# Optimization experiments

Hardware: AMD Instinct MI355X
Metric: run time of the kernel (lower is better)

The kernel has to match this reference:

```python
import jax, jax.numpy as jnp
import numpy as np

L, D, B, S = 131072, 512, 512, 512


def setup_inputs() -> dict:
    key = jax.random.key(0)
    k0, k1, k2, k3 = jax.random.split(key, 4)
    stdv = 1.0 / np.sqrt(D).astype(np.float32)
    inp = jax.random.normal(k0, (B, D), jnp.float32)
    labels = jax.random.normal(k1, (L, D), jnp.float32) * 0.05  # aggregated label embeddings 'v'
    weight = jax.random.uniform(k2, (L, D), jnp.float32, -stdv, stdv)  # refinement vectors 'u'
    alpha = jnp.zeros((1, D), jnp.float32)
    beta = jnp.zeros((1, D), jnp.float32)
    bias = jnp.zeros((L,), jnp.float32)
    shortlist = jax.random.randint(k3, (B, S), 0, L, dtype=jnp.int64)
    return {"input": inp, "labels": labels, "weight": weight,
            "alpha": alpha, "beta": beta, "bias": bias, "shortlist": shortlist}


def reference(input, labels, weight, alpha, beta, bias, shortlist):
    # sigmoid-gated combine of refinement vector u and label embedding v: [L, D]
    lbl_clf = jax.nn.sigmoid(alpha) * weight + jax.nn.sigmoid(beta) * labels
    # shortlist gather: [B, S, D] and [B, S]
    clf = lbl_clf[shortlist]
    b = bias[shortlist]
    # per-sample batched dot products: [B, S]
    out = jnp.einsum('bd,bsd->bs', input, clf) + b
    return out
```

## Files before the change

kernel.cpp:

```cpp
#include <hip/hip_runtime.h>


#define D_DIM 512
#define S_DIM 512

__global__ __launch_bounds__(256, 4)
void combine_uv_kernel(
    const float* __restrict__ input,
    const float* __restrict__ labels,
    const float* __restrict__ weight,
    const float* __restrict__ alpha,
    const float* __restrict__ beta,
    const float* __restrict__ bias,
    const int* __restrict__ shortlist,
    float* __restrict__ out)
{
    __shared__ float ga[D_DIM];
    __shared__ float gb[D_DIM];
    __shared__ int   sl[64];
    __shared__ float bb[64];

    const int b   = blockIdx.x;
    const int s0  = blockIdx.y * 64;
    const int tid = threadIdx.x;

    for (int d = tid; d < D_DIM; d += 256) {
        float x  = input[b * D_DIM + d];
        float sa = 1.0f / (1.0f + __expf(-alpha[d]));
        float sb = 1.0f / (1.0f + __expf(-beta[d]));
        ga[d] = x * sa;
        gb[d] = x * sb;
    }
    if (tid < 64) {
        const int l = shortlist[b * S_DIM + s0 + tid];
        sl[tid] = l;
        bb[tid] = bias[l];
    }
    __syncthreads();

    const int wave = tid >> 6;
    const int lane = tid & 63;
    const int g    = lane >> 4;
    const int m    = lane & 15;

    const float4* gaf = (const float4*)ga;
    const float4* gbf = (const float4*)gb;

    #pragma unroll
    for (int i = 0; i < 4; ++i) {
        const int    si = wave * 16 + i * 4 + g;
        const size_t l  = (size_t)sl[si];
        const float4* wrow = (const float4*)(weight + l * D_DIM);
        const float4* vrow = (const float4*)(labels + l * D_DIM);

        float4 wd[8], vd[8];
        #pragma unroll
        for (int k = 0; k < 8; ++k) wd[k] = wrow[m + 16 * k];
        #pragma unroll
        for (int k = 0; k < 8; ++k) vd[k] = vrow[m + 16 * k];

        float acc = 0.0f;
        #pragma unroll
        for (int k = 0; k < 8; ++k) {
            const float4 a = gaf[m + 16 * k];
            acc += wd[k].x * a.x + wd[k].y * a.y + wd[k].z * a.z + wd[k].w * a.w;
        }
        #pragma unroll
        for (int k = 0; k < 8; ++k) {
            const float4 c = gbf[m + 16 * k];
            acc += vd[k].x * c.x + vd[k].y * c.y + vd[k].z * c.z + vd[k].w * c.w;
        }

        acc += __shfl_xor(acc, 8, 64);
        acc += __shfl_xor(acc, 4, 64);
        acc += __shfl_xor(acc, 2, 64);
        acc += __shfl_xor(acc, 1, 64);

        if (m == 0) out[b * S_DIM + s0 + si] = acc + bb[si];
    }
}

extern "C" void kernel_launch(void* const* d_in, const int* in_sizes, int n_in,
                              void* d_out, int out_size, void* d_ws, size_t ws_size,
                              hipStream_t stream) {
    const float* input     = (const float*)d_in[0];
    const float* labels    = (const float*)d_in[1];
    const float* weight    = (const float*)d_in[2];
    const float* alpha     = (const float*)d_in[3];
    const float* beta      = (const float*)d_in[4];
    const float* bias      = (const float*)d_in[5];
    const int* shortlist   = (const int*)d_in[6];
    float* out             = (float*)d_out;

    const int B = 512;
    const int S = 512;
    dim3 grid(B, S / 64);
    dim3 block(256);
    combine_uv_kernel<<<grid, block, 0, stream>>>(
        input, labels, weight, alpha, beta, bias, shortlist, out);
}
```

Baseline: 567.1 us.

## Invert shortlist gather to label-major order via counting sort for row reuse

Builds a histogram, prefix scan and bucket fill of shortlist entries so each label's weight and label rows are loaded once and reused across every (batch, slot) pair that references them. Sample-major gathers of 4KB rows per pair are replaced by a streaming read over all labels plus gathers of the small precomputed gated-input matrices, which should stay cache-resident. This adds six extra launches, global atomics, workspace usage, and a serial per-wave inner loop with dependent index loads whose latency may limit throughput.

```diff
diff --git a/kernel.cpp b/kernel.cpp
--- a/kernel.cpp
+++ b/kernel.cpp
@@ -1,82 +1,141 @@
 #include <hip/hip_runtime.h>
 
 
+#define L_DIM 131072
 #define D_DIM 512
+#define B_DIM 512
 #define S_DIM 512
+#define NREF  (B_DIM * S_DIM)
 
-__global__ __launch_bounds__(256, 4)
-void combine_uv_kernel(
-    const float* __restrict__ input,
-    const float* __restrict__ labels,
-    const float* __restrict__ weight,
-    const float* __restrict__ alpha,
-    const float* __restrict__ beta,
-    const float* __restrict__ bias,
-    const int* __restrict__ shortlist,
-    float* __restrict__ out)
-{
-    __shared__ float ga[D_DIM];
-    __shared__ float gb[D_DIM];
-    __shared__ int   sl[64];
-    __shared__ float bb[64];
+#define WS_GA     0
+#define WS_GB     (1u << 20)
+#define WS_COUNTS (2u << 20)
+#define WS_STARTS ((2u << 20) + (512u << 10))
+#define WS_CURSOR (3u << 20)
+#define WS_BSUM   ((3u << 20) + (512u << 10))
+#define WS_BOFF   ((3u << 20) + (512u << 10) + 4096)
+#define WS_IDX    (4u << 20)
 
-    const int b   = blockIdx.x;
-    const int s0  = blockIdx.y * 64;
+__global__ void gates_kernel(const float* __restrict__ input,
+                             const float* __restrict__ alpha,
+                             const float* __restrict__ beta,
+                             float* __restrict__ ga, float* __restrict__ gb,
+                             int* __restrict__ counts) {
+    const int b = blockIdx.x, tid = threadIdx.x;
+    for (int d = tid; d < D_DIM; d += 256) {
+        const float x  = input[b * D_DIM + d];
+        const float sa = 1.0f / (1.0f + __expf(-alpha[d]));
+        const float sb = 1.0f / (1.0f + __expf(-beta[d]));
+        ga[b * D_DIM + d] = x * sa;
+        gb[b * D_DIM + d] = x * sb;
+    }
+    counts[b * 256 + tid] = 0;
+}
+
+__global__ void hist_kernel(const int* __restrict__ shortlist, int* __restrict__ counts) {
+    const int i = blockIdx.x * 256 + threadIdx.x;
+    atomicAdd(&counts[shortlist[i]], 1);
+}
+
+__global__ void scan1_kernel(const int* __restrict__ counts, int* __restrict__ bsum) {
+    __shared__ int s[256];
     const int tid = threadIdx.x;
+    s[tid] = counts[blockIdx.x * 256 + tid];
+    __syncthreads();
+    for (int off = 128; off > 0; off >>= 1) {
+        if (tid < off) s[tid] += s[tid + off];
+        __syncthreads();
+    }
+    if (tid == 0) bsum[blockIdx.x] = s[0];
+}
 
-    for (int d = tid; d < D_DIM; d += 256) {
-        float x  = input[b * D_DIM + d];
-        float sa = 1.0f / (1.0f + __expf(-alpha[d]));
-        float sb = 1.0f / (1.0f + __expf(-beta[d]));
-        ga[d] = x * sa;
-        gb[d] = x * sb;
+__global__ void scan2_kernel(const int* __restrict__ bsum, int* __restrict__ boff) {
+    __shared__ int s[512];
+    const int tid = threadIdx.x;
+    const int own = bsum[tid];
+    s[tid] = own;
+    __syncthreads();
+    for (int off = 1; off < 512; off <<= 1) {
+        const int v = (tid >= off) ? s[tid - off] : 0;
+        __syncthreads();
+        s[tid] += v;
+        __syncthreads();
     }
-    if (tid < 64) {
-        const int l = shortlist[b * S_DIM + s0 + tid];
-        sl[tid] = l;
-        bb[tid] = bias[l];
+    boff[tid] = s[tid] - own;
+}
+
+__global__ void scan3_kernel(const int* __restrict__ counts, const int* __restrict__ boff,
+                             int* __restrict__ starts, int* __restrict__ cursor) {
+    __shared__ int s[256];
+    const int tid = threadIdx.x;
+    const int i   = blockIdx.x * 256 + tid;
+    const int own = counts[i];
+    s[tid] = own;
+    __syncthreads();
+    for (int off = 1; off < 256; off <<= 1) {
+        const int v = (tid >= off) ? s[tid - off] : 0;
+        __syncthreads();
+        s[tid] += v;
+        __syncthreads();
     }
-    __syncthreads();
+    const int st = boff[blockIdx.x] + s[tid] - own;
+    starts[i] = st;
+    cursor[i] = st;
+}
 
-    const int wave = tid >> 6;
-    const int lane = tid & 63;
-    const int g    = lane >> 4;
-    const int m    = lane & 15;
+__global__ void fill_kernel(const int* __restrict__ shortlist, int* __restrict__ cursor,
+                            unsigned* __restrict__ idx) {
+    const int i = blockIdx.x * 256 + threadIdx.x;
+    const int l = shortlist[i];
+    const int pos = atomicAdd(&cursor[l], 1);
+    idx[pos] = (unsigned)i;
+}
 
-    const float4* gaf = (const float4*)ga;
-    const float4* gbf = (const float4*)gb;
+__global__ __launch_bounds__(256)
+void main_kernel(const float* __restrict__ weight, const float* __restrict__ labels,
+                 const float* __restrict__ bias,
+                 const float* __restrict__ ga, const float* __restrict__ gb,
+                 const int* __restrict__ starts, const int* __restrict__ counts,
+                 const unsigned* __restrict__ idx, float* __restrict__ out) {
+    const int wave = threadIdx.x >> 6;
+    const int lane = threadIdx.x & 63;
+    const int row0 = (blockIdx.x * 4 + wave) * 16;
 
-    #pragma unroll
-    for (int i = 0; i < 4; ++i) {
-        const int    si = wave * 16 + i * 4 + g;
-        const size_t l  = (size_t)sl[si];
-        const float4* wrow = (const float4*)(weight + l * D_DIM);
-        const float4* vrow = (const float4*)(labels + l * D_DIM);
+    const float4* __restrict__ Wf = (const float4*)weight;
+    const float4* __restrict__ Vf = (const float4*)labels;
+    const float4* __restrict__ GA = (const float4*)ga;
+    const float4* __restrict__ GB = (const float4*)gb;
 
-        float4 wd[8], vd[8];
-        #pragma unroll
-        for (int k = 0; k < 8; ++k) wd[k] = wrow[m + 16 * k];
-        #pragma unroll
-        for (int k = 0; k < 8; ++k) vd[k] = vrow[m + 16 * k];
+    for (int r = 0; r < 16; ++r) {
+        const int l = row0 + r;
+        const int n = counts[l];
+        if (n == 0) continue;
+        const int   st = starts[l];
+        const float bl = bias[l];
 
-        float acc = 0.0f;
-        #pragma unroll
-        for (int k = 0; k < 8; ++k) {
-            const float4 a = gaf[m + 16 * k];
-            acc += wd[k].x * a.x + wd[k].y * a.y + wd[k].z * a.z + wd[k].w * a.w;
+        const int base = l * 128 + lane * 2;
+        const float4 w0 = Wf[base], w1 = Wf[base + 1];
+        const float4 v0 = Vf[base], v1 = Vf[base + 1];
+
+        for (int j = 0; j < n; ++j) {
+            const unsigned e = idx[st + j];
+            const int bb = (int)(e >> 9);
+            const int ss = (int)(e & 511u);
+            const int gbase = bb * 128 + lane * 2;
+            const float4 A0 = GA[gbase], A1 = GA[gbase + 1];
+            const float4 B0 = GB[gbase], B1 = GB[gbase + 1];
+
+            float acc = w0.x * A0.x + w0.y * A0.y + w0.z * A0.z + w0.w * A0.w
+                      + w1.x * A1.x + w1.y * A1.y + w1.z * A1.z + w1.w * A1.w
+                      + v0.x * B0.x + v0.y * B0.y + v0.z * B0.z + v0.w * B0.w
+                      + v1.x * B1.x + v1.y * B1.y + v1.z * B1.z + v1.w * B1.w;
+
+            #pragma unroll
+            for (int off = 32; off > 0; off >>= 1)
+                acc += __shfl_xor(acc, off, 64);
+
+            if (lane == 0) out[bb * S_DIM + ss] = acc + bl;
         }
-        #pragma unroll
-        for (int k = 0; k < 8; ++k) {
-            const float4 c = gbf[m + 16 * k];
-            acc += vd[k].x * c.x + vd[k].y * c.y + vd[k].z * c.z + vd[k].w * c.w;
-        }
-
-        acc += __shfl_xor(acc, 8, 64);
-        acc += __shfl_xor(acc, 4, 64);
-        acc += __shfl_xor(acc, 2, 64);
-        acc += __shfl_xor(acc, 1, 64);
-
-        if (m == 0) out[b * S_DIM + s0 + si] = acc + bb[si];
     }
 }
 
@@ -92,10 +151,22 @@
     const int* shortlist   = (const int*)d_in[6];
     float* out             = (float*)d_out;
 
-    const int B = 512;
-    const int S = 512;
-    dim3 grid(B, S / 64);
-    dim3 block(256);
-    combine_uv_kernel<<<grid, block, 0, stream>>>(
-        input, labels, weight, alpha, beta, bias, shortlist, out);
+    char* ws = (char*)d_ws;
+    float*    ga     = (float*)(ws + WS_GA);
+    float*    gb     = (float*)(ws + WS_GB);
+    int*      counts = (int*)(ws + WS_COUNTS);
+    int*      starts = (int*)(ws + WS_STARTS);
+    int*      cursor = (int*)(ws + WS_CURSOR);
+    int*      bsum   = (int*)(ws + WS_BSUM);
+    int*      boff   = (int*)(ws + WS_BOFF);
+    unsigned* idx    = (unsigned*)(ws + WS_IDX);
+
+    gates_kernel<<<dim3(512), dim3(256), 0, stream>>>(input, alpha, beta, ga, gb, counts);
+    hist_kernel <<<dim3(1024), dim3(256), 0, stream>>>(shortlist, counts);
+    scan1_kernel<<<dim3(512), dim3(256), 0, stream>>>(counts, bsum);
+    scan2_kernel<<<dim3(1),   dim3(512), 0, stream>>>(bsum, boff);
+    scan3_kernel<<<dim3(512), dim3(256), 0, stream>>>(counts, boff, starts, cursor);
+    fill_kernel <<<dim3(1024), dim3(256), 0, stream>>>(shortlist, cursor, idx);
+    main_kernel <<<dim3(2048), dim3(256), 0, stream>>>(weight, labels, bias, ga, gb,
+                                                       starts, counts, idx, out);
 }
```

Result: slower. 582.4 us (+2.7%).
